# Kernel tuning notes

Measured on AMD Instinct MI355X. Metric: run time of the kernel, lower is better.

Reference implementation:

```python
import jax, jax.numpy as jnp
import numpy as np

B, N, E, H = 8, 1024, 768, 12
HD = E // H

def setup_inputs() -> dict:
    key = jax.random.key(0)
    k1, k2, k3, k4, k5 = jax.random.split(key, 5)
    s = 0.02
    return {
        'query': jax.random.normal(k1, (B, N, E), dtype=jnp.float32),
        'qkv_w': jax.random.normal(k2, (3 * E, E), dtype=jnp.float32) * s,
        'qkv_b': jax.random.normal(k3, (3 * E,), dtype=jnp.float32) * s,
        'out_w': jax.random.normal(k4, (E, E), dtype=jnp.float32) * s,
        'out_b': jax.random.normal(k5, (E,), dtype=jnp.float32) * s,
    }

def reference(query, qkv_w, qkv_b, out_w, out_b):
    b, n, e = query.shape
    scale = HD ** -0.5
    # torch Linear: x @ W^T + b
    qkv = query @ qkv_w.T + qkv_b              # [B,N,3E]
    qkv = qkv.reshape(b, n, 3, H, HD)
    q = qkv[:, :, 0].transpose(0, 2, 1, 3)     # [B,H,N,hd]
    k = qkv[:, :, 1].transpose(0, 2, 1, 3)
    v = qkv[:, :, 2].transpose(0, 2, 1, 3)
    attn = jnp.einsum('bhqd,bhkd->bhqk', q, k) * scale
    attn = jax.nn.softmax(attn, axis=-1)
    x = jnp.einsum('bhqk,bhkd->bhqd', attn, v)  # [B,H,N,hd]
    x = x.transpose(0, 2, 1, 3).reshape(b, n, e)
    return x @ out_w.T + out_b
```

## Files before the change

kernel.cpp:

```cpp
#include <hip/hip_runtime.h>
#include <cstdint>
#include <cstddef>

#define QSCALE 0.18033688011112042f

typedef __bf16 bf16x8 __attribute__((ext_vector_type(8)));
typedef __bf16 bf16x4 __attribute__((ext_vector_type(4)));
typedef short short4v __attribute__((ext_vector_type(4)));
typedef float floatx4 __attribute__((ext_vector_type(4)));

static __device__ __forceinline__ uint16_t f2bf(float f) {
    uint32_t u = __builtin_bit_cast(uint32_t, f);
    u += 0x7FFFu + ((u >> 16) & 1u);
    return (uint16_t)(u >> 16);
}

static __device__ __forceinline__ void st_bf16(uint16_t* p, float f) {
    *(__bf16*)p = (__bf16)f;
}

static __device__ __forceinline__ bf16x8 ld_frag(const uint16_t* p) {
    uint4 u = *(const uint4*)p;
    return __builtin_bit_cast(bf16x8, u);
}

static __device__ __forceinline__ void async_lds16(const uint16_t* g, uint16_t* l) {
    __builtin_amdgcn_global_load_lds(
        (const __attribute__((address_space(1))) void*)g,
        (__attribute__((address_space(3))) void*)l,
        16, 0, 0);
}

static __device__ __forceinline__ size_t qk_swz(int bh, int idx, int hd) {
    return (size_t)bh * 65536 + (size_t)(idx >> 4) * 1024 + (size_t)(hd >> 5) * 512
         + (size_t)((hd & 31) >> 3) * 128 + (size_t)(idx & 15) * 8 + (hd & 7);
}
static __device__ __forceinline__ size_t v_swz(int bh, int hd, int key) {
    return (size_t)bh * 65536 + (size_t)(key >> 6) * 4096 + (size_t)(hd >> 4) * 1024
         + (size_t)((key >> 4) & 3) * 256 + (size_t)((key >> 2) & 3) * 64
         + (size_t)(hd & 15) * 4 + (key & 3);
}

__global__ __launch_bounds__(256) void cast3_kernel(
    const float* __restrict__ a, uint16_t* __restrict__ da, int na8,
    const float* __restrict__ b, uint16_t* __restrict__ db, int nb8,
    const float* __restrict__ c, uint16_t* __restrict__ dc, int nc8)
{
    int i = blockIdx.x * 256 + threadIdx.x;
    const float* src; uint16_t* dst; int idx;
    if (i < na8)                { src = a; dst = da; idx = i; }
    else if (i < na8 + nb8)     { src = b; dst = db; idx = i - na8; }
    else if (i < na8 + nb8 + nc8){ src = c; dst = dc; idx = i - na8 - nb8; }
    else return;
    const float4* p = (const float4*)src + (size_t)2 * idx;
    float4 x = p[0], y = p[1];
    uint32_t w0 = (uint32_t)f2bf(x.x) | ((uint32_t)f2bf(x.y) << 16);
    uint32_t w1 = (uint32_t)f2bf(x.z) | ((uint32_t)f2bf(x.w) << 16);
    uint32_t w2 = (uint32_t)f2bf(y.x) | ((uint32_t)f2bf(y.y) << 16);
    uint32_t w3 = (uint32_t)f2bf(y.z) | ((uint32_t)f2bf(y.w) << 16);
    uint4 v; v.x = w0; v.y = w1; v.z = w2; v.w = w3;
    *((uint4*)dst + idx) = v;
}

__global__ __launch_bounds__(256) void gemm_qkv_kernel(
    const uint16_t* __restrict__ X,
    const uint16_t* __restrict__ W,
    const float* __restrict__ bias,
    uint16_t* __restrict__ Qs, uint16_t* __restrict__ Ks, uint16_t* __restrict__ Vs)
{
    __shared__ __align__(16) uint16_t As[128 * 32];
    __shared__ __align__(16) uint16_t Bs[128 * 32];
    const int tid = threadIdx.x;
    const int wave = tid >> 6, lane = tid & 63;
    const int L = lane & 15, quad = lane >> 4;
    const int wM = (wave >> 1) * 64, wN = (wave & 1) * 64;
    const int bm = blockIdx.x * 128;
    const int bn = blockIdx.y * 128;

    floatx4 zero4 = {0.f, 0.f, 0.f, 0.f};
    floatx4 acc[4][4];
    #pragma unroll
    for (int i = 0; i < 4; ++i)
        #pragma unroll
        for (int j = 0; j < 4; ++j) acc[i][j] = zero4;

    const int srow = tid >> 2;
    const int scol = ((tid & 3) ^ ((srow >> 1) & 3)) * 8;
    const uint16_t* xp0 = X + (size_t)(bm + srow) * 768 + scol;
    const uint16_t* xp1 = xp0 + (size_t)64 * 768;
    const uint16_t* wp0 = W + (size_t)(bn + srow) * 768 + scol;
    const uint16_t* wp1 = wp0 + (size_t)64 * 768;
    uint16_t* lA0 = As + wave * 512;
    uint16_t* lA1 = As + 2048 + wave * 512;
    uint16_t* lB0 = Bs + wave * 512;
    uint16_t* lB1 = Bs + 2048 + wave * 512;

    const int cq = (quad ^ ((L >> 1) & 3)) * 8;

    for (int k0 = 0; k0 < 768; k0 += 32) {
        __syncthreads();
        async_lds16(xp0 + k0, lA0);
        async_lds16(xp1 + k0, lA1);
        async_lds16(wp0 + k0, lB0);
        async_lds16(wp1 + k0, lB1);
        __syncthreads();
        bf16x8 af[4], bfr[4];
        #pragma unroll
        for (int mi = 0; mi < 4; ++mi) af[mi]  = ld_frag(&As[(wM + mi * 16 + L) * 32 + cq]);
        #pragma unroll
        for (int ni = 0; ni < 4; ++ni) bfr[ni] = ld_frag(&Bs[(wN + ni * 16 + L) * 32 + cq]);
        #pragma unroll
        for (int mi = 0; mi < 4; ++mi)
            #pragma unroll
            for (int ni = 0; ni < 4; ++ni)
                acc[mi][ni] = __builtin_amdgcn_mfma_f32_16x16x32_bf16(
                    af[mi], bfr[ni], acc[mi][ni], 0, 0, 0);
    }

    const int part = bn / 768;
    #pragma unroll
    for (int ni = 0; ni < 4; ++ni) {
        int col = bn + wN + ni * 16 + L;
        int c = col - part * 768;
        int h = c >> 6, hd = c & 63;
        float bv = bias[col];
        #pragma unroll
        for (int mi = 0; mi < 4; ++mi) {
            #pragma unroll
            for (int r = 0; r < 4; ++r) {
                int m = bm + wM + mi * 16 + quad * 4 + r;
                int b = m >> 10, ns = m & 1023;
                int bh = b * 12 + h;
                float v = acc[mi][ni][r] + bv;
                if (part == 0)      st_bf16(&Qs[qk_swz(bh, ns, hd)], v * QSCALE);
                else if (part == 1) st_bf16(&Ks[qk_swz(bh, ns, hd)], v);
                else                st_bf16(&Vs[v_swz(bh, hd, ns)], v);
            }
        }
    }
}

__global__ __launch_bounds__(256) void attn_kernel(
    const uint16_t* __restrict__ Qs,
    const uint16_t* __restrict__ Ks,
    const uint16_t* __restrict__ Vs,
    uint16_t* __restrict__ Ob)
{
    const int tid = threadIdx.x;
    const int wave = tid >> 6, lane = tid & 63;
    const int L = lane & 15, quad = lane >> 4;
    const int bh = blockIdx.x;
    const int qt = blockIdx.y;
    const int b = bh / 12, h = bh - b * 12;
    const int q0 = qt * 128 + wave * 32;

    floatx4 zero4 = {0.f, 0.f, 0.f, 0.f};

    const uint16_t* qbase = Qs + (size_t)bh * 65536 + (size_t)lane * 8;
    bf16x8 aq[2][2];
    #pragma unroll
    for (int st = 0; st < 2; ++st) {
        const uint16_t* qp = qbase + (size_t)(qt * 8 + wave * 2 + st) * 1024;
        aq[st][0] = ld_frag(qp);
        aq[st][1] = ld_frag(qp + 512);
    }

    floatx4 accO[2][4];
    #pragma unroll
    for (int st = 0; st < 2; ++st)
        #pragma unroll
        for (int t = 0; t < 4; ++t) accO[st][t] = zero4;
    float lacc[2] = {0.f, 0.f};

    const uint16_t* kbase = Ks + (size_t)bh * 65536 + (size_t)lane * 8;
    const uint16_t* vbase = Vs + (size_t)bh * 65536 + (size_t)lane * 4;

    for (int j = 0; j < 16; ++j) {
        bf16x8 ka[4][2];
        #pragma unroll
        for (int kc = 0; kc < 4; ++kc) {
            const uint16_t* kp = kbase + (size_t)(j * 4 + kc) * 1024;
            ka[kc][0] = ld_frag(kp);
            ka[kc][1] = ld_frag(kp + 512);
        }
        short4v va[4][4];
        const uint16_t* vp = vbase + (size_t)j * 4096;
        #pragma unroll
        for (int t = 0; t < 4; ++t)
            #pragma unroll
            for (int kc = 0; kc < 4; ++kc)
                va[kc][t] = *(const short4v*)(vp + t * 1024 + kc * 256);

        floatx4 c[2][4];
        #pragma unroll
        for (int st = 0; st < 2; ++st)
            #pragma unroll
            for (int kc = 0; kc < 4; ++kc) {
                floatx4 z = zero4;
                z = __builtin_amdgcn_mfma_f32_16x16x32_bf16(ka[kc][0], aq[st][0], z, 0, 0, 0);
                z = __builtin_amdgcn_mfma_f32_16x16x32_bf16(ka[kc][1], aq[st][1], z, 0, 0, 0);
                c[st][kc] = z;
            }

        short4v pb[2][4];
        #pragma unroll
        for (int st = 0; st < 2; ++st)
            #pragma unroll
            for (int kc = 0; kc < 4; ++kc) {
                float p0 = __builtin_amdgcn_exp2f(c[st][kc][0]);
                float p1 = __builtin_amdgcn_exp2f(c[st][kc][1]);
                float p2 = __builtin_amdgcn_exp2f(c[st][kc][2]);
                float p3 = __builtin_amdgcn_exp2f(c[st][kc][3]);
                lacc[st] += (p0 + p1) + (p2 + p3);
                bf16x4 t4;
                t4.x = (__bf16)p0; t4.y = (__bf16)p1;
                t4.z = (__bf16)p2; t4.w = (__bf16)p3;
                pb[st][kc] = __builtin_bit_cast(short4v, t4);
            }

        #pragma unroll
        for (int st = 0; st < 2; ++st)
            #pragma unroll
            for (int t = 0; t < 4; ++t)
                #pragma unroll
                for (int kc = 0; kc < 4; ++kc)
                    accO[st][t] = __builtin_amdgcn_mfma_f32_16x16x16bf16_1k(
                        va[kc][t], pb[st][kc], accO[st][t], 0, 0, 0);
    }

    #pragma unroll
    for (int st = 0; st < 2; ++st) {
        float sum = lacc[st];
        sum += __shfl_xor(sum, 16);
        sum += __shfl_xor(sum, 32);
        float inv = 1.f / sum;
        uint16_t* orow = Ob + ((size_t)b * 1024 + q0 + st * 16 + L) * 768 + h * 64 + quad * 4;
        #pragma unroll
        for (int t = 0; t < 4; ++t) {
            bf16x4 o4;
            o4.x = (__bf16)(accO[st][t][0] * inv);
            o4.y = (__bf16)(accO[st][t][1] * inv);
            o4.z = (__bf16)(accO[st][t][2] * inv);
            o4.w = (__bf16)(accO[st][t][3] * inv);
            *(uint2*)(orow + t * 16) = __builtin_bit_cast(uint2, o4);
        }
    }
}

__global__ __launch_bounds__(256) void gemm_out_kernel(
    const uint16_t* __restrict__ X,
    const uint16_t* __restrict__ W,
    const float* __restrict__ bias,
    float* __restrict__ out)
{
    __shared__ __align__(16) uint16_t As[128 * 32];
    __shared__ __align__(16) uint16_t Bs[64 * 32];
    const int tid = threadIdx.x;
    const int wave = tid >> 6, lane = tid & 63;
    const int L = lane & 15, quad = lane >> 4;
    const int wM = (wave >> 1) * 64, wN = (wave & 1) * 32;
    const int bm = blockIdx.x * 128;
    const int bn = blockIdx.y * 64;

    floatx4 zero4 = {0.f, 0.f, 0.f, 0.f};
    floatx4 acc[4][2];
    #pragma unroll
    for (int i = 0; i < 4; ++i)
        #pragma unroll
        for (int j = 0; j < 2; ++j) acc[i][j] = zero4;

    const int srow = tid >> 2;
    const int scol = ((tid & 3) ^ ((srow >> 1) & 3)) * 8;
    const uint16_t* xp0 = X + (size_t)(bm + srow) * 768 + scol;
    const uint16_t* xp1 = xp0 + (size_t)64 * 768;
    const uint16_t* wp0 = W + (size_t)(bn + srow) * 768 + scol;
    uint16_t* lA0 = As + wave * 512;
    uint16_t* lA1 = As + 2048 + wave * 512;
    uint16_t* lB0 = Bs + wave * 512;

    const int cq = (quad ^ ((L >> 1) & 3)) * 8;

    for (int k0 = 0; k0 < 768; k0 += 32) {
        __syncthreads();
        async_lds16(xp0 + k0, lA0);
        async_lds16(xp1 + k0, lA1);
        async_lds16(wp0 + k0, lB0);
        __syncthreads();
        bf16x8 af[4], bfr[2];
        #pragma unroll
        for (int mi = 0; mi < 4; ++mi) af[mi]  = ld_frag(&As[(wM + mi * 16 + L) * 32 + cq]);
        #pragma unroll
        for (int ni = 0; ni < 2; ++ni) bfr[ni] = ld_frag(&Bs[(wN + ni * 16 + L) * 32 + cq]);
        #pragma unroll
        for (int mi = 0; mi < 4; ++mi)
            #pragma unroll
            for (int ni = 0; ni < 2; ++ni)
                acc[mi][ni] = __builtin_amdgcn_mfma_f32_16x16x32_bf16(
                    af[mi], bfr[ni], acc[mi][ni], 0, 0, 0);
    }

    #pragma unroll
    for (int ni = 0; ni < 2; ++ni) {
        int col = bn + wN + ni * 16 + L;
        float bv = bias[col];
        #pragma unroll
        for (int mi = 0; mi < 4; ++mi)
            #pragma unroll
            for (int r = 0; r < 4; ++r) {
                int m = bm + wM + mi * 16 + quad * 4 + r;
                out[(size_t)m * 768 + col] = acc[mi][ni][r] + bv;
            }
    }
}

extern "C" void kernel_launch(void* const* d_in, const int* in_sizes, int n_in,
                              void* d_out, int out_size, void* d_ws, size_t ws_size,
                              hipStream_t stream) {
    const float* query = (const float*)d_in[0];
    const float* qkv_w = (const float*)d_in[1];
    const float* qkv_b = (const float*)d_in[2];
    const float* out_w = (const float*)d_in[3];
    const float* out_b = (const float*)d_in[4];
    float* out = (float*)d_out;

    uint8_t* ws = (uint8_t*)d_ws;
    uint16_t* Xb  = (uint16_t*)(ws);
    uint16_t* W1b = (uint16_t*)(ws + 12582912);
    uint16_t* W2b = (uint16_t*)(ws + 16121856);
    uint16_t* Qsw = (uint16_t*)(ws + 17301504);
    uint16_t* Ksw = (uint16_t*)(ws + 29884416);
    uint16_t* Vsw = (uint16_t*)(ws + 42467328);
    uint16_t* Ab  = Xb;

    cast3_kernel<<<4224, 256, 0, stream>>>(query, Xb, 786432,
                                           qkv_w, W1b, 221184,
                                           out_w, W2b, 73728);
    gemm_qkv_kernel<<<dim3(64, 18), 256, 0, stream>>>(Xb, W1b, qkv_b, Qsw, Ksw, Vsw);
    attn_kernel<<<dim3(96, 8), 256, 0, stream>>>(Qsw, Ksw, Vsw, Ab);
    gemm_out_kernel<<<dim3(64, 12), 256, 0, stream>>>(Ab, W2b, out_b, out);
}
```

Before: 193.5 us.

## Double-buffer LDS tiles in QKV and output projection GEMMs

Both projection GEMMs now use two LDS buffers for the A and B tiles. The loop is unrolled by two so that the async global-to-LDS load of the next K-slice is issued before the MFMA work on the current slice, rather than only after a barrier. The aim is to hide global load latency behind the matrix math. In exchange, LDS use per block doubles, which may lower occupancy.

Result: slower. 204.5 us (+5.7%).

```diff
diff --git a/kernel.cpp b/kernel.cpp
--- a/kernel.cpp
+++ b/kernel.cpp
@@ -68,8 +68,10 @@
     const float* __restrict__ bias,
     uint16_t* __restrict__ Qs, uint16_t* __restrict__ Ks, uint16_t* __restrict__ Vs)
 {
-    __shared__ __align__(16) uint16_t As[128 * 32];
-    __shared__ __align__(16) uint16_t Bs[128 * 32];
+    __shared__ __align__(16) uint16_t As0[128 * 32];
+    __shared__ __align__(16) uint16_t As1[128 * 32];
+    __shared__ __align__(16) uint16_t Bs0[128 * 32];
+    __shared__ __align__(16) uint16_t Bs1[128 * 32];
     const int tid = threadIdx.x;
     const int wave = tid >> 6, lane = tid & 63;
     const int L = lane & 15, quad = lane >> 4;
@@ -90,32 +92,45 @@
     const uint16_t* xp1 = xp0 + (size_t)64 * 768;
     const uint16_t* wp0 = W + (size_t)(bn + srow) * 768 + scol;
     const uint16_t* wp1 = wp0 + (size_t)64 * 768;
-    uint16_t* lA0 = As + wave * 512;
-    uint16_t* lA1 = As + 2048 + wave * 512;
-    uint16_t* lB0 = Bs + wave * 512;
-    uint16_t* lB1 = Bs + 2048 + wave * 512;
+    const int lofs0 = wave * 512, lofs1 = 2048 + wave * 512;
 
     const int cq = (quad ^ ((L >> 1) & 3)) * 8;
 
-    for (int k0 = 0; k0 < 768; k0 += 32) {
+#define QKV_STAGE(kk, Adst, Bdst)                    \
+    do {                                             \
+        async_lds16(xp0 + (kk), &Adst[lofs0]);       \
+        async_lds16(xp1 + (kk), &Adst[lofs1]);       \
+        async_lds16(wp0 + (kk), &Bdst[lofs0]);       \
+        async_lds16(wp1 + (kk), &Bdst[lofs1]);       \
+    } while (0)
+
+#define QKV_COMPUTE(Asrc, Bsrc)                                                        \
+    do {                                                                               \
+        bf16x8 af[4], bfr[4];                                                          \
+        _Pragma("unroll")                                                              \
+        for (int mi = 0; mi < 4; ++mi) af[mi]  = ld_frag(&Asrc[(wM + mi * 16 + L) * 32 + cq]); \
+        _Pragma("unroll")                                                              \
+        for (int ni = 0; ni < 4; ++ni) bfr[ni] = ld_frag(&Bsrc[(wN + ni * 16 + L) * 32 + cq]); \
+        _Pragma("unroll")                                                              \
+        for (int mi = 0; mi < 4; ++mi)                                                 \
+            _Pragma("unroll")                                                          \
+            for (int ni = 0; ni < 4; ++ni)                                             \
+                acc[mi][ni] = __builtin_amdgcn_mfma_f32_16x16x32_bf16(                 \
+                    af[mi], bfr[ni], acc[mi][ni], 0, 0, 0);                            \
+    } while (0)
+
+    QKV_STAGE(0, As0, Bs0);
+    for (int it = 0; it < 12; ++it) {
+        const int kb = it * 64;
         __syncthreads();
-        async_lds16(xp0 + k0, lA0);
-        async_lds16(xp1 + k0, lA1);
-        async_lds16(wp0 + k0, lB0);
-        async_lds16(wp1 + k0, lB1);
+        QKV_STAGE(kb + 32, As1, Bs1);
+        QKV_COMPUTE(As0, Bs0);
         __syncthreads();
-        bf16x8 af[4], bfr[4];
-        #pragma unroll
-        for (int mi = 0; mi < 4; ++mi) af[mi]  = ld_frag(&As[(wM + mi * 16 + L) * 32 + cq]);
-        #pragma unroll
-        for (int ni = 0; ni < 4; ++ni) bfr[ni] = ld_frag(&Bs[(wN + ni * 16 + L) * 32 + cq]);
-        #pragma unroll
-        for (int mi = 0; mi < 4; ++mi)
-            #pragma unroll
-            for (int ni = 0; ni < 4; ++ni)
-                acc[mi][ni] = __builtin_amdgcn_mfma_f32_16x16x32_bf16(
-                    af[mi], bfr[ni], acc[mi][ni], 0, 0, 0);
-    }
+        if (it < 11) QKV_STAGE(kb + 64, As0, Bs0);
+        QKV_COMPUTE(As1, Bs1);
+    }
+#undef QKV_STAGE
+#undef QKV_COMPUTE
 
     const int part = bn / 768;
     #pragma unroll
@@ -253,8 +268,10 @@
     const float* __restrict__ bias,
     float* __restrict__ out)
 {
-    __shared__ __align__(16) uint16_t As[128 * 32];
-    __shared__ __align__(16) uint16_t Bs[64 * 32];
+    __shared__ __align__(16) uint16_t As0[128 * 32];
+    __shared__ __align__(16) uint16_t As1[128 * 32];
+    __shared__ __align__(16) uint16_t Bs0[64 * 32];
+    __shared__ __align__(16) uint16_t Bs1[64 * 32];
     const int tid = threadIdx.x;
     const int wave = tid >> 6, lane = tid & 63;
     const int L = lane & 15, quad = lane >> 4;
@@ -274,30 +291,44 @@
     const uint16_t* xp0 = X + (size_t)(bm + srow) * 768 + scol;
     const uint16_t* xp1 = xp0 + (size_t)64 * 768;
     const uint16_t* wp0 = W + (size_t)(bn + srow) * 768 + scol;
-    uint16_t* lA0 = As + wave * 512;
-    uint16_t* lA1 = As + 2048 + wave * 512;
-    uint16_t* lB0 = Bs + wave * 512;
+    const int lofs0 = wave * 512, lofs1 = 2048 + wave * 512;
 
     const int cq = (quad ^ ((L >> 1) & 3)) * 8;
 
-    for (int k0 = 0; k0 < 768; k0 += 32) {
+#define OUT_STAGE(kk, Adst, Bdst)                    \
+    do {                                             \
+        async_lds16(xp0 + (kk), &Adst[lofs0]);       \
+        async_lds16(xp1 + (kk), &Adst[lofs1]);       \
+        async_lds16(wp0 + (kk), &Bdst[lofs0]);       \
+    } while (0)
+
+#define OUT_COMPUTE(Asrc, Bsrc)                                                        \
+    do {                                                                               \
+        bf16x8 af[4], bfr[2];                                                          \
+        _Pragma("unroll")                                                              \
+        for (int mi = 0; mi < 4; ++mi) af[mi]  = ld_frag(&Asrc[(wM + mi * 16 + L) * 32 + cq]); \
+        _Pragma("unroll")                                                              \
+        for (int ni = 0; ni < 2; ++ni) bfr[ni] = ld_frag(&Bsrc[(wN + ni * 16 + L) * 32 + cq]); \
+        _Pragma("unroll")                                                              \
+        for (int mi = 0; mi < 4; ++mi)                                                 \
+            _Pragma("unroll")                                                          \
+            for (int ni = 0; ni < 2; ++ni)                                             \
+                acc[mi][ni] = __builtin_amdgcn_mfma_f32_16x16x32_bf16(                 \
+                    af[mi], bfr[ni], acc[mi][ni], 0, 0, 0);                            \
+    } while (0)
+
+    OUT_STAGE(0, As0, Bs0);
+    for (int it = 0; it < 12; ++it) {
+        const int kb = it * 64;
         __syncthreads();
-        async_lds16(xp0 + k0, lA0);
-        async_lds16(xp1 + k0, lA1);
-        async_lds16(wp0 + k0, lB0);
+        OUT_STAGE(kb + 32, As1, Bs1);
+        OUT_COMPUTE(As0, Bs0);
         __syncthreads();
-        bf16x8 af[4], bfr[2];
-        #pragma unroll
-        for (int mi = 0; mi < 4; ++mi) af[mi]  = ld_frag(&As[(wM + mi * 16 + L) * 32 + cq]);
-        #pragma unroll
-        for (int ni = 0; ni < 2; ++ni) bfr[ni] = ld_frag(&Bs[(wN + ni * 16 + L) * 32 + cq]);
-        #pragma unroll
-        for (int mi = 0; mi < 4; ++mi)
-            #pragma unroll
-            for (int ni = 0; ni < 2; ++ni)
-                acc[mi][ni] = __builtin_amdgcn_mfma_f32_16x16x32_bf16(
-                    af[mi], bfr[ni], acc[mi][ni], 0, 0, 0);
-    }
+        if (it < 11) OUT_STAGE(kb + 64, As0, Bs0);
+        OUT_COMPUTE(As1, Bs1);
+    }
+#undef OUT_STAGE
+#undef OUT_COMPUTE
 
     #pragma unroll
     for (int ni = 0; ni < 2; ++ni) {
```
